# Kernel tuning notes

Hardware: AMD Instinct MI355X
Metric: run time of the kernel (lower is better)

The kernel has to match this reference:

```python
import jax, jax.numpy as jnp
import numpy as np

NUM_HEADS = 16
THETA = 10000.0


def _apply_rope(x, pos):
    # x: [b, h, t, d_k], pos: [t] int
    d = x.shape[-1]
    inv_freq = THETA ** (-jnp.arange(0, d, 2, dtype=jnp.float32) / d)  # [d/2]
    ang = pos.astype(jnp.float32)[:, None] * inv_freq                  # [t, d/2]
    cos, sin = jnp.cos(ang), jnp.sin(ang)
    x1, x2 = x[..., ::2], x[..., 1::2]
    r1 = x1 * cos - x2 * sin
    r2 = x1 * sin + x2 * cos
    return jnp.stack([r1, r2], axis=-1).reshape(x.shape)


def setup_inputs() -> dict:
    key = jax.random.key(0)
    k1, k2, k3 = jax.random.split(key, 3)
    b, t, dm = 4, 2048, 2048
    in_features = jax.random.normal(k1, (b, t, dm), dtype=jnp.float32)
    token_positions = jnp.arange(t, dtype=jnp.int64)
    W_qkv = jax.random.normal(k2, (3 * dm, dm), dtype=jnp.float32) * 0.02
    W_o = jax.random.normal(k3, (dm, dm), dtype=jnp.float32) * 0.02
    return {"in_features": in_features, "token_positions": token_positions,
            "W_qkv": W_qkv, "W_o": W_o}


def reference(in_features, token_positions, W_qkv, W_o):
    b, t, dm = in_features.shape
    h = NUM_HEADS
    dk = dm // h
    # fused QKV projection (Linear: y = x W^T)
    qkv = in_features @ W_qkv.T                       # [b, t, 3*dm]
    q, k, v = jnp.split(qkv, 3, axis=-1)
    def to_heads(x):
        return x.reshape(b, t, h, dk).transpose(0, 2, 1, 3)  # [b, h, t, dk]
    q, k, v = to_heads(q), to_heads(k), to_heads(v)
    q = _apply_rope(q, token_positions)
    k = _apply_rope(k, token_positions)
    # causal SDPA
    scale = 1.0 / np.sqrt(dk).astype(np.float32)
    scores = jnp.einsum('bhqd,bhkd->bhqk', q, k) * scale
    causal = jnp.tril(jnp.ones((t, t), dtype=bool))
    scores = jnp.where(causal, scores, jnp.finfo(scores.dtype).min)
    attn = jax.nn.softmax(scores, axis=-1)
    out = jnp.einsum('bhqk,bhkd->bhqd', attn, v)      # [b, h, t, dk]
    out = out.transpose(0, 2, 1, 3).reshape(b, t, dm)
    return out @ W_o.T
```

## Files before the change

### kernel.cpp

```cpp
#include <hip/hip_runtime.h>

typedef unsigned short u16;
typedef __attribute__((ext_vector_type(8))) short s8v;
typedef __attribute__((ext_vector_type(8))) __bf16 bf8;
typedef __attribute__((ext_vector_type(4))) float f4v;

#define GLB(p) ((const __attribute__((address_space(1))) void*)(p))
#define LDS(p) ((__attribute__((address_space(3))) void*)(p))

static __device__ __forceinline__ float b2f(u16 u) {
    union { unsigned int i; float f; } v; v.i = ((unsigned int)u) << 16; return v.f;
}
static __device__ __forceinline__ u16 f2b(float f) {
    union { float f; unsigned int i; } v; v.f = f;
    v.i += 0x7fffu + ((v.i >> 16) & 1u);
    return (u16)(v.i >> 16);
}

__global__ __launch_bounds__(256) void k_conv(const float* __restrict__ X,
                                              const float* __restrict__ Wq,
                                              const float* __restrict__ Wo,
                                              u16* __restrict__ Xb,
                                              u16* __restrict__ Wqb,
                                              u16* __restrict__ Wob) {
    int i = blockIdx.x * 256 + threadIdx.x;
    const float* in; u16* out; int off;
    if (i < 4194304)      { in = X;  out = Xb;  off = i; }
    else if (i < 7340032) { in = Wq; out = Wqb; off = i - 4194304; }
    else                  { in = Wo; out = Wob; off = i - 7340032; }
    float4 v = ((const float4*)in)[off];
    union { u16 u[4]; unsigned long long ll; } o;
    o.u[0] = f2b(v.x); o.u[1] = f2b(v.y); o.u[2] = f2b(v.z); o.u[3] = f2b(v.w);
    ((unsigned long long*)out)[off] = o.ll;
}

template<int MODE>
__global__ __launch_bounds__(512, 2) void k_gemm_bt(
    const u16* __restrict__ A, const u16* __restrict__ B,
    int K, int N, int gx,
    u16* __restrict__ Qb, u16* __restrict__ Kb, u16* __restrict__ Vt,
    float* __restrict__ Cf, const int* __restrict__ pos)
{
    extern __shared__ __align__(16) u16 Ls[];

    const int t    = threadIdx.x;
    const int lane = t & 63;
    const int wid  = t >> 6;
    const int wm = wid >> 2, wn = wid & 3;
    const int la = lane & 15, lb = lane >> 4;

    const int bid = (int)blockIdx.x;
    const int id2 = (bid & 7) * ((int)gridDim.x >> 3) + (bid >> 3);
    const int bx = id2 % gx, by = id2 / gx;
    const long arow0 = (long)by * 256;
    const long brow0 = (long)bx * 256;

    const int sr = t >> 3;
    const int sg = (t & 7) ^ (sr & 7);
    const u16* Asrc = A + (arow0 + sr) * (long)K + sg * 8;
    const u16* Bsrc = B + (brow0 + sr) * (long)K + sg * 8;
    const long K64 = 64 * (long)K, K128 = 128 * (long)K;
    u16* ldst = Ls + t * 8;

#define STG(q_, op_, h_, kt_) do {                                              \
        const u16* s_ = ((op_) ? Bsrc : Asrc) + (h_) * K128 + (long)(kt_) * 64; \
        u16* d_ = ldst + (q_) * 32768 + (op_) * 16384 + (h_) * 8192;            \
        __builtin_amdgcn_global_load_lds(GLB(s_),       LDS(d_),        16, 0, 0); \
        __builtin_amdgcn_global_load_lds(GLB(s_ + K64), LDS(d_ + 4096), 16, 0, 0); \
    } while (0)
#define RD(off) (*(const bf8*)(Ls + (off)))

    f4v acc[8][4];
#pragma unroll
    for (int m = 0; m < 8; m++)
#pragma unroll
        for (int n = 0; n < 4; n++) acc[m][n] = (f4v){0.f, 0.f, 0.f, 0.f};

    const int r7 = la & 7;
    const int gA0 = (lb ^ r7) * 8;
    const int gA1 = ((lb ^ r7) ^ 4) * 8;
    const int aRow = wm * 8192 + la * 64;
    const int bRow = 16384 + (wn >> 1) * 8192 + ((wn & 1) * 64 + la) * 64;

    const int NKT = K >> 6;
    STG(0, 0, 0, 0); STG(0, 0, 1, 0); STG(0, 1, 0, 0); STG(0, 1, 1, 0);
    asm volatile("s_waitcnt vmcnt(0)" ::: "memory");
    __builtin_amdgcn_s_barrier();

    for (int X = 0; X < NKT; ++X) {
        const int D = (X & 1) << 15;
        const int q = (X + 1) & 1;
        const int S = (X + 1 < NKT) ? X + 1 : NKT - 1;
        bf8 aR[4][2], b0[2][2], b1[2][2];

#pragma unroll
        for (int mi = 0; mi < 4; mi++) {
            aR[mi][0] = RD(D + aRow + mi * 1024 + gA0);
            aR[mi][1] = RD(D + aRow + mi * 1024 + gA1);
        }
#pragma unroll
        for (int nl = 0; nl < 2; nl++) {
            b0[nl][0] = RD(D + bRow + nl * 1024 + gA0);
            b0[nl][1] = RD(D + bRow + nl * 1024 + gA1);
        }
        STG(q, 0, 0, S); STG(q, 0, 1, S); STG(q, 1, 0, S); STG(q, 1, 1, S);
        __builtin_amdgcn_s_barrier();
        __builtin_amdgcn_s_setprio(1);
#pragma unroll
        for (int mi = 0; mi < 4; mi++)
#pragma unroll
            for (int nl = 0; nl < 2; nl++) {
                acc[mi][nl] = __builtin_amdgcn_mfma_f32_16x16x32_bf16(aR[mi][0], b0[nl][0], acc[mi][nl], 0, 0, 0);
                acc[mi][nl] = __builtin_amdgcn_mfma_f32_16x16x32_bf16(aR[mi][1], b0[nl][1], acc[mi][nl], 0, 0, 0);
            }
        __builtin_amdgcn_s_setprio(0);

#pragma unroll
        for (int nl = 0; nl < 2; nl++) {
            b1[nl][0] = RD(D + bRow + (2 + nl) * 1024 + gA0);
            b1[nl][1] = RD(D + bRow + (2 + nl) * 1024 + gA1);
        }
        __builtin_amdgcn_s_barrier();
        __builtin_amdgcn_s_setprio(1);
#pragma unroll
        for (int mi = 0; mi < 4; mi++)
#pragma unroll
            for (int nl = 0; nl < 2; nl++) {
                acc[mi][2 + nl] = __builtin_amdgcn_mfma_f32_16x16x32_bf16(aR[mi][0], b1[nl][0], acc[mi][2 + nl], 0, 0, 0);
                acc[mi][2 + nl] = __builtin_amdgcn_mfma_f32_16x16x32_bf16(aR[mi][1], b1[nl][1], acc[mi][2 + nl], 0, 0, 0);
            }
        __builtin_amdgcn_s_setprio(0);

#pragma unroll
        for (int mi = 0; mi < 4; mi++) {
            aR[mi][0] = RD(D + aRow + (4 + mi) * 1024 + gA0);
            aR[mi][1] = RD(D + aRow + (4 + mi) * 1024 + gA1);
        }
        __builtin_amdgcn_s_barrier();
        __builtin_amdgcn_s_setprio(1);
#pragma unroll
        for (int mi = 0; mi < 4; mi++)
#pragma unroll
            for (int nl = 0; nl < 2; nl++) {
                acc[4 + mi][2 + nl] = __builtin_amdgcn_mfma_f32_16x16x32_bf16(aR[mi][0], b1[nl][0], acc[4 + mi][2 + nl], 0, 0, 0);
                acc[4 + mi][2 + nl] = __builtin_amdgcn_mfma_f32_16x16x32_bf16(aR[mi][1], b1[nl][1], acc[4 + mi][2 + nl], 0, 0, 0);
            }
        __builtin_amdgcn_s_setprio(0);

        asm volatile("s_waitcnt vmcnt(0)" ::: "memory");
        __builtin_amdgcn_s_barrier();
        __builtin_amdgcn_s_setprio(1);
#pragma unroll
        for (int mi = 0; mi < 4; mi++)
#pragma unroll
            for (int nl = 0; nl < 2; nl++) {
                acc[4 + mi][nl] = __builtin_amdgcn_mfma_f32_16x16x32_bf16(aR[mi][0], b0[nl][0], acc[4 + mi][nl], 0, 0, 0);
                acc[4 + mi][nl] = __builtin_amdgcn_mfma_f32_16x16x32_bf16(aR[mi][1], b0[nl][1], acc[4 + mi][nl], 0, 0, 0);
            }
        __builtin_amdgcn_s_setprio(0);
    }
#undef STG
#undef RD

    if (MODE == 1) {
#pragma unroll
        for (int mi = 0; mi < 8; mi++)
#pragma unroll
            for (int ni = 0; ni < 4; ni++) {
                const long grow0 = arow0 + wm * 128 + mi * 16 + lb * 4;
                const int  gcol  = (int)brow0 + wn * 64 + ni * 16 + la;
#pragma unroll
                for (int i = 0; i < 4; i++)
                    Cf[(grow0 + i) * (long)N + gcol] = acc[mi][ni][i];
            }
        return;
    }

    __syncthreads();
    const int part = (int)(brow0 >> 11);
    const int colp = (int)brow0 & 2047;
    const int h0   = colp >> 7;
    const int bidx = (int)(arow0 >> 11);
    const int t0   = (int)arow0 & 2047;

    if (part == 2) {
#pragma unroll
        for (int mi = 0; mi < 8; mi++)
#pragma unroll
            for (int ni = 0; ni < 4; ni++) {
                const int tlb = wm * 128 + mi * 16 + lb * 4;
                const int dl  = wn * 64 + ni * 16 + la;
#pragma unroll
                for (int i2 = 0; i2 < 2; i2++) {
                    unsigned int pk = (unsigned int)f2b(acc[mi][ni][i2 * 2])
                                    | ((unsigned int)f2b(acc[mi][ni][i2 * 2 + 1]) << 16);
                    *(unsigned int*)(Ls + dl * 264 + tlb + i2 * 2) = pk;
                }
            }
        __syncthreads();
#pragma unroll
        for (int j = 0; j < 16; j++) {
            const int dl = j * 16 + wid * 2 + (lane >> 5);
            const int c  = lane & 31;
            bf8 v = *(const bf8*)(Ls + dl * 264 + c * 8);
            const long bh = (long)(bidx * 16 + h0 + (dl >> 7));
            *(bf8*)(Vt + (bh << 18) + ((long)(dl & 127) << 11) + t0 + c * 8) = v;
        }
    } else {
        u16* dst = (part == 0) ? Qb : Kb;
#pragma unroll
        for (int mi = 0; mi < 8; mi++)
#pragma unroll
            for (int ni = 0; ni < 4; ni++) {
                const int tlb = wm * 128 + mi * 16 + lb * 4;
                const int dl  = wn * 64 + ni * 16 + la;
#pragma unroll
                for (int i = 0; i < 4; i++)
                    Ls[(tlb + i) * 264 + dl] = f2b(acc[mi][ni][i]);
            }
        __syncthreads();
        const int c = t & 15;
        float invf[4];
#pragma unroll
        for (int p2 = 0; p2 < 4; p2++)
            invf[p2] = exp2f((float)(c * 4 + p2) * -0.20762050593046014f);
#pragma unroll
        for (int j = 0; j < 16; j++) {
            const int R  = j * 32 + (t >> 4);
            const int tl = R >> 1, hh = R & 1;
            s8v v = *(const s8v*)(Ls + tl * 264 + hh * 128 + c * 8);
            const float pf = (float)pos[t0 + tl];
            union { u16 u[8]; s8v v; } ov;
#pragma unroll
            for (int p2 = 0; p2 < 4; p2++) {
                float x1 = b2f((u16)v[2 * p2]);
                float x2 = b2f((u16)v[2 * p2 + 1]);
                float sn, cs;
                __sincosf(pf * invf[p2], &sn, &cs);
                ov.u[2 * p2]     = f2b(x1 * cs - x2 * sn);
                ov.u[2 * p2 + 1] = f2b(x1 * sn + x2 * cs);
            }
            const long bh = (long)(bidx * 16 + h0 + hh);
            *(s8v*)(dst + ((bh << 11) + t0 + tl) * 128 + c * 8) = ov.v;
        }
    }
}

__global__ __launch_bounds__(256) void k_attn(const u16* __restrict__ Qb,
                                              const u16* __restrict__ Kb,
                                              const u16* __restrict__ Vt,
                                              u16* __restrict__ Ob)
{
    extern __shared__ __align__(16) u16 Sm[];
    u16* KsD = Sm;
    u16* VsD = Sm + 16384;
    u16* PlD = Sm + 32768;

    const int tid  = threadIdx.x;
    const int lane = tid & 63;
    const int w    = tid >> 6;
    const int la = lane & 15, lb = lane >> 4;
    const int qg = 15 - ((int)blockIdx.x >> 6);
    const int bh = blockIdx.x & 63;
    const long base = (long)bh << 18;
    const int qt = qg * 4 + w;
    const int q0 = qt * 32;
    const int n32 = qt + 1;
    const int NT = qg * 2 + 2;
    const float scale = 0.08838834764831845f;

    bf8 qf[2][4];
#pragma unroll
    for (int m = 0; m < 2; m++)
#pragma unroll
        for (int kb = 0; kb < 4; kb++)
            qf[m][kb] = *(const bf8*)(Qb + base + (long)(q0 + m * 16 + la) * 128 + kb * 32 + lb * 8);

    f4v o[2][8];
#pragma unroll
    for (int m = 0; m < 2; m++)
#pragma unroll
        for (int n = 0; n < 8; n++) o[m][n] = (f4v){0.f, 0.f, 0.f, 0.f};
    float lst[2][4];
#pragma unroll
    for (int m = 0; m < 2; m++)
#pragma unroll
        for (int i = 0; i < 4; i++) lst[m][i] = 0.f;

    char* Pb = (char*)(PlD + w * 1024);

    const int krow = tid >> 4;
    const int kgr  = (tid & 15) ^ (krow & 7);
    const int vrow = tid >> 3;
    const int vgr  = (tid & 7) ^ (vrow & 7);

#define STAGE(buf, jt_) do {                                                         \
        const int kv0_ = (jt_) * 64;                                                \
        _Pragma("unroll")                                                           \
        for (int i_ = 0; i_ < 4; i_++) {                                            \
            __builtin_amdgcn_global_load_lds(                                       \
                GLB(Kb + base + (long)(kv0_ + i_ * 16 + krow) * 128 + kgr * 8),     \
                LDS(KsD + (buf) * 8192 + i_ * 2048 + tid * 8), 16, 0, 0);           \
            __builtin_amdgcn_global_load_lds(                                       \
                GLB(Vt + base + (long)(i_ * 32 + vrow) * 2048 + kv0_ + vgr * 8),    \
                LDS(VsD + (buf) * 8192 + i_ * 2048 + tid * 8), 16, 0, 0);           \
        }                                                                           \
    } while (0)

    STAGE(0, 0);

    for (int jt = 0; jt < NT; ++jt) {
        const int buf = jt & 1;
        asm volatile("s_waitcnt vmcnt(0)" ::: "memory");
        __builtin_amdgcn_s_barrier();
        if (jt + 1 < NT) STAGE(buf ^ 1, jt + 1);

        const u16* KsB = KsD + buf * 8192;
        const u16* VsB = VsD + buf * 8192;

#pragma unroll
        for (int h = 0; h < 2; h++) {
            const int j32 = jt * 2 + h;
            if (j32 < n32) {
                f4v s[2][2];
                s[0][0] = s[0][1] = s[1][0] = s[1][1] = (f4v){0.f, 0.f, 0.f, 0.f};
#pragma unroll
                for (int n = 0; n < 2; n++) {
                    const int rr = h * 32 + n * 16 + la;
#pragma unroll
                    for (int kb = 0; kb < 4; kb++) {
                        bf8 kf = *(const bf8*)(KsB + rr * 128 + (((kb * 4 + lb) ^ (la & 7)) * 8));
                        s[0][n] = __builtin_amdgcn_mfma_f32_16x16x32_bf16(qf[0][kb], kf, s[0][n], 0, 0, 0);
                        s[1][n] = __builtin_amdgcn_mfma_f32_16x16x32_bf16(qf[1][kb], kf, s[1][n], 0, 0, 0);
                    }
                }

                bf8 vf[8];
#pragma unroll
                for (int nO = 0; nO < 8; nO++) {
                    const int rv = nO * 16 + la;
                    vf[nO] = *(const bf8*)(VsB + rv * 64 + (((h * 4 + lb) ^ (la & 7)) * 8));
                }

                const bool diag = (j32 == qt);
                float p[2][2][4];
#pragma unroll
                for (int m = 0; m < 2; m++)
#pragma unroll
                    for (int n = 0; n < 2; n++)
#pragma unroll
                        for (int i = 0; i < 4; i++) {
                            float v = __expf(fmaf(s[m][n][i], scale, -8.0f));
                            if (diag && (n * 16 + la) > (m * 16 + lb * 4 + i)) v = 0.f;
                            p[m][n][i] = v;
                            lst[m][i] += v;
                        }

#pragma unroll
                for (int m = 0; m < 2; m++)
#pragma unroll
                    for (int n = 0; n < 2; n++)
#pragma unroll
                        for (int i = 0; i < 4; i++) {
                            const int row = m * 16 + lb * 4 + i;
                            const int colb = (n * 16 + la) * 2;
                            *(u16*)(Pb + row * 64 + (colb ^ ((row & 3) << 4))) = f2b(p[m][n][i]);
                        }
                bf8 pa[2];
#pragma unroll
                for (int am = 0; am < 2; am++) {
                    const int row = am * 16 + la;
                    pa[am] = *(const bf8*)(Pb + row * 64 + ((lb * 16) ^ ((row & 3) << 4)));
                }
#pragma unroll
                for (int nO = 0; nO < 8; nO++) {
                    o[0][nO] = __builtin_amdgcn_mfma_f32_16x16x32_bf16(pa[0], vf[nO], o[0][nO], 0, 0, 0);
                    o[1][nO] = __builtin_amdgcn_mfma_f32_16x16x32_bf16(pa[1], vf[nO], o[1][nO], 0, 0, 0);
                }
            }
        }
        __builtin_amdgcn_s_barrier();
    }
#undef STAGE

    float linv[2][4];
#pragma unroll
    for (int m = 0; m < 2; m++)
#pragma unroll
        for (int i = 0; i < 4; i++) {
            float l = lst[m][i];
            l += __shfl_xor(l, 1);
            l += __shfl_xor(l, 2);
            l += __shfl_xor(l, 4);
            l += __shfl_xor(l, 8);
            linv[m][i] = 1.0f / l;
        }

    const int b = bh >> 4, h = bh & 15;
#pragma unroll
    for (int m = 0; m < 2; m++)
#pragma unroll
        for (int nO = 0; nO < 8; nO++)
#pragma unroll
            for (int i = 0; i < 4; i++) {
                const int row = q0 + m * 16 + lb * 4 + i;
                const int d = nO * 16 + la;
                Ob[((long)(b * 2048 + row) << 11) + h * 128 + d] = f2b(o[m][nO][i] * linv[m][i]);
            }
}

extern "C" void kernel_launch(void* const* d_in, const int* in_sizes, int n_in,
                              void* d_out, int out_size, void* d_ws, size_t ws_size,
                              hipStream_t stream)
{
    const float* X    = (const float*)d_in[0];
    const int*   pos  = (const int*)d_in[1];
    const float* Wqkv = (const float*)d_in[2];
    const float* Wo   = (const float*)d_in[3];
    float* out = (float*)d_out;

    char* ws = (char*)d_ws;
    u16* Xb    = (u16*)(ws + 0);
    u16* Wqkvb = (u16*)(ws + 33554432);
    u16* Wob   = (u16*)(ws + 58720256);
    u16* Qb    = (u16*)(ws + 67108864);
    u16* Kb    = (u16*)(ws + 100663296);
    u16* Vt    = (u16*)(ws + 134217728);
    u16* Ob    = (u16*)(ws + 167772160);

    k_conv<<<32768, 256, 0, stream>>>(X, Wqkv, Wo, Xb, Wqkvb, Wob);
    k_gemm_bt<0><<<768, 512, 135168, stream>>>(Xb, Wqkvb, 2048, 6144, 24, Qb, Kb, Vt, nullptr, pos);
    k_attn<<<1024, 256, 73728, stream>>>(Qb, Kb, Vt, Ob);
    k_gemm_bt<1><<<256, 512, 131072, stream>>>(Ob, Wob, 2048, 2048, 8, nullptr, nullptr, nullptr, out, nullptr);
}
```

Measured before the change: 392.9 us.

## Simplify GEMM main loop to single-barrier double buffer with full fragment loads

Replaces the four-phase ping-pong GEMM K-loop, which interleaved partial LDS fragment reads with MFMA groups across several barriers, with a simpler scheme. Each iteration waits for the previous prefetch, does one barrier, issues the next tile's global-to-LDS loads, reads all A/B fragments, then runs all 64 MFMAs. It also drops a trailing barrier in the attention loop. This cuts barrier count and simplifies scheduling, but uses more registers for fragments, overlaps LDS reads with MFMA less, and removing the attention barrier could introduce an LDS race.

```diff
diff --git a/kernel.cpp b/kernel.cpp
--- a/kernel.cpp
+++ b/kernel.cpp
@@ -84,81 +84,38 @@
 
     const int NKT = K >> 6;
     STG(0, 0, 0, 0); STG(0, 0, 1, 0); STG(0, 1, 0, 0); STG(0, 1, 1, 0);
-    asm volatile("s_waitcnt vmcnt(0)" ::: "memory");
-    __builtin_amdgcn_s_barrier();
 
     for (int X = 0; X < NKT; ++X) {
-        const int D = (X & 1) << 15;
-        const int q = (X + 1) & 1;
-        const int S = (X + 1 < NKT) ? X + 1 : NKT - 1;
-        bf8 aR[4][2], b0[2][2], b1[2][2];
-
-#pragma unroll
-        for (int mi = 0; mi < 4; mi++) {
-            aR[mi][0] = RD(D + aRow + mi * 1024 + gA0);
-            aR[mi][1] = RD(D + aRow + mi * 1024 + gA1);
-        }
-#pragma unroll
-        for (int nl = 0; nl < 2; nl++) {
-            b0[nl][0] = RD(D + bRow + nl * 1024 + gA0);
-            b0[nl][1] = RD(D + bRow + nl * 1024 + gA1);
-        }
-        STG(q, 0, 0, S); STG(q, 0, 1, S); STG(q, 1, 0, S); STG(q, 1, 1, S);
-        __builtin_amdgcn_s_barrier();
-        __builtin_amdgcn_s_setprio(1);
-#pragma unroll
-        for (int mi = 0; mi < 4; mi++)
-#pragma unroll
-            for (int nl = 0; nl < 2; nl++) {
-                acc[mi][nl] = __builtin_amdgcn_mfma_f32_16x16x32_bf16(aR[mi][0], b0[nl][0], acc[mi][nl], 0, 0, 0);
-                acc[mi][nl] = __builtin_amdgcn_mfma_f32_16x16x32_bf16(aR[mi][1], b0[nl][1], acc[mi][nl], 0, 0, 0);
-            }
-        __builtin_amdgcn_s_setprio(0);
-
-#pragma unroll
-        for (int nl = 0; nl < 2; nl++) {
-            b1[nl][0] = RD(D + bRow + (2 + nl) * 1024 + gA0);
-            b1[nl][1] = RD(D + bRow + (2 + nl) * 1024 + gA1);
-        }
-        __builtin_amdgcn_s_barrier();
-        __builtin_amdgcn_s_setprio(1);
-#pragma unroll
-        for (int mi = 0; mi < 4; mi++)
-#pragma unroll
-            for (int nl = 0; nl < 2; nl++) {
-                acc[mi][2 + nl] = __builtin_amdgcn_mfma_f32_16x16x32_bf16(aR[mi][0], b1[nl][0], acc[mi][2 + nl], 0, 0, 0);
-                acc[mi][2 + nl] = __builtin_amdgcn_mfma_f32_16x16x32_bf16(aR[mi][1], b1[nl][1], acc[mi][2 + nl], 0, 0, 0);
-            }
-        __builtin_amdgcn_s_setprio(0);
-
-#pragma unroll
-        for (int mi = 0; mi < 4; mi++) {
-            aR[mi][0] = RD(D + aRow + (4 + mi) * 1024 + gA0);
-            aR[mi][1] = RD(D + aRow + (4 + mi) * 1024 + gA1);
-        }
-        __builtin_amdgcn_s_barrier();
-        __builtin_amdgcn_s_setprio(1);
-#pragma unroll
-        for (int mi = 0; mi < 4; mi++)
-#pragma unroll
-            for (int nl = 0; nl < 2; nl++) {
-                acc[4 + mi][2 + nl] = __builtin_amdgcn_mfma_f32_16x16x32_bf16(aR[mi][0], b1[nl][0], acc[4 + mi][2 + nl], 0, 0, 0);
-                acc[4 + mi][2 + nl] = __builtin_amdgcn_mfma_f32_16x16x32_bf16(aR[mi][1], b1[nl][1], acc[4 + mi][2 + nl], 0, 0, 0);
-            }
-        __builtin_amdgcn_s_setprio(0);
-
         asm volatile("s_waitcnt vmcnt(0)" ::: "memory");
         __builtin_amdgcn_s_barrier();
+        if (X + 1 < NKT) {
+            const int q = (X + 1) & 1;
+            STG(q, 0, 0, X + 1); STG(q, 0, 1, X + 1);
+            STG(q, 1, 0, X + 1); STG(q, 1, 1, X + 1);
+        }
+
+        const int D = (X & 1) << 15;
+        bf8 aF[8][2], bF[4][2];
+#pragma unroll
+        for (int mi = 0; mi < 8; mi++) aF[mi][0] = RD(D + aRow + mi * 1024 + gA0);
+#pragma unroll
+        for (int ni = 0; ni < 4; ni++) bF[ni][0] = RD(D + bRow + ni * 1024 + gA0);
+#pragma unroll
+        for (int mi = 0; mi < 8; mi++) aF[mi][1] = RD(D + aRow + mi * 1024 + gA1);
+#pragma unroll
+        for (int ni = 0; ni < 4; ni++) bF[ni][1] = RD(D + bRow + ni * 1024 + gA1);
+
         __builtin_amdgcn_s_setprio(1);
 #pragma unroll
-        for (int mi = 0; mi < 4; mi++)
-#pragma unroll
-            for (int nl = 0; nl < 2; nl++) {
-                acc[4 + mi][nl] = __builtin_amdgcn_mfma_f32_16x16x32_bf16(aR[mi][0], b0[nl][0], acc[4 + mi][nl], 0, 0, 0);
-                acc[4 + mi][nl] = __builtin_amdgcn_mfma_f32_16x16x32_bf16(aR[mi][1], b0[nl][1], acc[4 + mi][nl], 0, 0, 0);
-            }
+        for (int kk = 0; kk < 2; kk++)
+#pragma unroll
+            for (int mi = 0; mi < 8; mi++)
+#pragma unroll
+                for (int ni = 0; ni < 4; ni++)
+                    acc[mi][ni] = __builtin_amdgcn_mfma_f32_16x16x32_bf16(aF[mi][kk], bF[ni][kk], acc[mi][ni], 0, 0, 0);
         __builtin_amdgcn_s_setprio(0);
     }
+    asm volatile("s_waitcnt vmcnt(0)" ::: "memory");
 #undef STG
 #undef RD
 
@@ -379,7 +336,6 @@
                 }
             }
         }
-        __builtin_amdgcn_s_barrier();
     }
 #undef STAGE
 
```

Result: no change. 393.7 us (+0.2%).

## Load K/V fragments directly from global memory in attention, dropping LDS staging

Applied to the files above, without the earlier changes.

The attention kernel no longer stages K and V tiles into double-buffered shared memory with async global-to-LDS loads and block barriers. Each wave now reads its MFMA K and V fragments straight from global memory and walks its own causal range of 32-key tiles with no block-level synchronisation. This frees about 64KB of LDS per block to raise occupancy and removes barrier stalls between waves of uneven length. The cost is that the four waves of a block each fetch the same K/V data separately through the cache, with no software prefetch overlap.

```diff
diff --git a/kernel.cpp b/kernel.cpp
--- a/kernel.cpp
+++ b/kernel.cpp
@@ -251,10 +251,7 @@
                                               const u16* __restrict__ Vt,
                                               u16* __restrict__ Ob)
 {
-    extern __shared__ __align__(16) u16 Sm[];
-    u16* KsD = Sm;
-    u16* VsD = Sm + 16384;
-    u16* PlD = Sm + 32768;
+    __shared__ __align__(16) u16 Pl[4][1024];
 
     const int tid  = threadIdx.x;
     const int lane = tid & 63;
@@ -266,7 +263,6 @@
     const int qt = qg * 4 + w;
     const int q0 = qt * 32;
     const int n32 = qt + 1;
-    const int NT = qg * 2 + 2;
     const float scale = 0.08838834764831845f;
 
     bf8 qf[2][4];
@@ -287,101 +283,66 @@
 #pragma unroll
         for (int i = 0; i < 4; i++) lst[m][i] = 0.f;
 
-    char* Pb = (char*)(PlD + w * 1024);
-
-    const int krow = tid >> 4;
-    const int kgr  = (tid & 15) ^ (krow & 7);
-    const int vrow = tid >> 3;
-    const int vgr  = (tid & 7) ^ (vrow & 7);
-
-#define STAGE(buf, jt_) do {                                                         \
-        const int kv0_ = (jt_) * 64;                                                \
-        _Pragma("unroll")                                                           \
-        for (int i_ = 0; i_ < 4; i_++) {                                            \
-            __builtin_amdgcn_global_load_lds(                                       \
-                GLB(Kb + base + (long)(kv0_ + i_ * 16 + krow) * 128 + kgr * 8),     \
-                LDS(KsD + (buf) * 8192 + i_ * 2048 + tid * 8), 16, 0, 0);           \
-            __builtin_amdgcn_global_load_lds(                                       \
-                GLB(Vt + base + (long)(i_ * 32 + vrow) * 2048 + kv0_ + vgr * 8),    \
-                LDS(VsD + (buf) * 8192 + i_ * 2048 + tid * 8), 16, 0, 0);           \
-        }                                                                           \
-    } while (0)
-
-    STAGE(0, 0);
-
-    for (int jt = 0; jt < NT; ++jt) {
-        const int buf = jt & 1;
-        asm volatile("s_waitcnt vmcnt(0)" ::: "memory");
-        __builtin_amdgcn_s_barrier();
-        if (jt + 1 < NT) STAGE(buf ^ 1, jt + 1);
-
-        const u16* KsB = KsD + buf * 8192;
-        const u16* VsB = VsD + buf * 8192;
-
-#pragma unroll
-        for (int h = 0; h < 2; h++) {
-            const int j32 = jt * 2 + h;
-            if (j32 < n32) {
-                f4v s[2][2];
-                s[0][0] = s[0][1] = s[1][0] = s[1][1] = (f4v){0.f, 0.f, 0.f, 0.f};
-#pragma unroll
-                for (int n = 0; n < 2; n++) {
-                    const int rr = h * 32 + n * 16 + la;
-#pragma unroll
-                    for (int kb = 0; kb < 4; kb++) {
-                        bf8 kf = *(const bf8*)(KsB + rr * 128 + (((kb * 4 + lb) ^ (la & 7)) * 8));
-                        s[0][n] = __builtin_amdgcn_mfma_f32_16x16x32_bf16(qf[0][kb], kf, s[0][n], 0, 0, 0);
-                        s[1][n] = __builtin_amdgcn_mfma_f32_16x16x32_bf16(qf[1][kb], kf, s[1][n], 0, 0, 0);
-                    }
+    char* Pb = (char*)(Pl[w]);
+    const u16* Kg = Kb + base + (long)la * 128 + lb * 8;
+    const u16* Vg = Vt + base + (long)la * 2048 + lb * 8;
+
+    for (int j32 = 0; j32 < n32; ++j32) {
+        const int kv0 = j32 * 32;
+
+        bf8 vf[8];
+#pragma unroll
+        for (int nO = 0; nO < 8; nO++)
+            vf[nO] = *(const bf8*)(Vg + nO * 32768 + kv0);
+
+        f4v s[2][2];
+        s[0][0] = s[0][1] = s[1][0] = s[1][1] = (f4v){0.f, 0.f, 0.f, 0.f};
+#pragma unroll
+        for (int n = 0; n < 2; n++) {
+#pragma unroll
+            for (int kb = 0; kb < 4; kb++) {
+                bf8 kf = *(const bf8*)(Kg + (long)(kv0 + n * 16) * 128 + kb * 32);
+                s[0][n] = __builtin_amdgcn_mfma_f32_16x16x32_bf16(qf[0][kb], kf, s[0][n], 0, 0, 0);
+                s[1][n] = __builtin_amdgcn_mfma_f32_16x16x32_bf16(qf[1][kb], kf, s[1][n], 0, 0, 0);
+            }
+        }
+
+        const bool diag = (j32 == qt);
+        float p[2][2][4];
+#pragma unroll
+        for (int m = 0; m < 2; m++)
+#pragma unroll
+            for (int n = 0; n < 2; n++)
+#pragma unroll
+                for (int i = 0; i < 4; i++) {
+                    float v = __expf(fmaf(s[m][n][i], scale, -8.0f));
+                    if (diag && (n * 16 + la) > (m * 16 + lb * 4 + i)) v = 0.f;
+                    p[m][n][i] = v;
+                    lst[m][i] += v;
                 }
 
-                bf8 vf[8];
-#pragma unroll
-                for (int nO = 0; nO < 8; nO++) {
-                    const int rv = nO * 16 + la;
-                    vf[nO] = *(const bf8*)(VsB + rv * 64 + (((h * 4 + lb) ^ (la & 7)) * 8));
+#pragma unroll
+        for (int m = 0; m < 2; m++)
+#pragma unroll
+            for (int n = 0; n < 2; n++)
+#pragma unroll
+                for (int i = 0; i < 4; i++) {
+                    const int row = m * 16 + lb * 4 + i;
+                    const int colb = (n * 16 + la) * 2;
+                    *(u16*)(Pb + row * 64 + (colb ^ ((row & 3) << 4))) = f2b(p[m][n][i]);
                 }
-
-                const bool diag = (j32 == qt);
-                float p[2][2][4];
-#pragma unroll
-                for (int m = 0; m < 2; m++)
-#pragma unroll
-                    for (int n = 0; n < 2; n++)
-#pragma unroll
-                        for (int i = 0; i < 4; i++) {
-                            float v = __expf(fmaf(s[m][n][i], scale, -8.0f));
-                            if (diag && (n * 16 + la) > (m * 16 + lb * 4 + i)) v = 0.f;
-                            p[m][n][i] = v;
-                            lst[m][i] += v;
-                        }
-
-#pragma unroll
-                for (int m = 0; m < 2; m++)
-#pragma unroll
-                    for (int n = 0; n < 2; n++)
-#pragma unroll
-                        for (int i = 0; i < 4; i++) {
-                            const int row = m * 16 + lb * 4 + i;
-                            const int colb = (n * 16 + la) * 2;
-                            *(u16*)(Pb + row * 64 + (colb ^ ((row & 3) << 4))) = f2b(p[m][n][i]);
-                        }
-                bf8 pa[2];
-#pragma unroll
-                for (int am = 0; am < 2; am++) {
-                    const int row = am * 16 + la;
-                    pa[am] = *(const bf8*)(Pb + row * 64 + ((lb * 16) ^ ((row & 3) << 4)));
-                }
-#pragma unroll
-                for (int nO = 0; nO < 8; nO++) {
-                    o[0][nO] = __builtin_amdgcn_mfma_f32_16x16x32_bf16(pa[0], vf[nO], o[0][nO], 0, 0, 0);
-                    o[1][nO] = __builtin_amdgcn_mfma_f32_16x16x32_bf16(pa[1], vf[nO], o[1][nO], 0, 0, 0);
-                }
-            }
-        }
-        __builtin_amdgcn_s_barrier();
+        bf8 pa[2];
+#pragma unroll
+        for (int am = 0; am < 2; am++) {
+            const int row = am * 16 + la;
+            pa[am] = *(const bf8*)(Pb + row * 64 + ((lb * 16) ^ ((row & 3) << 4)));
+        }
+#pragma unroll
+        for (int nO = 0; nO < 8; nO++) {
+            o[0][nO] = __builtin_amdgcn_mfma_f32_16x16x32_bf16(pa[0], vf[nO], o[0][nO], 0, 0, 0);
+            o[1][nO] = __builtin_amdgcn_mfma_f32_16x16x32_bf16(pa[1], vf[nO], o[1][nO], 0, 0, 0);
+        }
     }
-#undef STAGE
 
     float linv[2][4];
 #pragma unroll
@@ -430,6 +391,6 @@
 
     k_conv<<<32768, 256, 0, stream>>>(X, Wqkv, Wo, Xb, Wqkvb, Wob);
     k_gemm_bt<0><<<768, 512, 135168, stream>>>(Xb, Wqkvb, 2048, 6144, 24, Qb, Kb, Vt, nullptr, pos);
-    k_attn<<<1024, 256, 73728, stream>>>(Qb, Kb, Vt, Ob);
+    k_attn<<<1024, 256, 0, stream>>>(Qb, Kb, Vt, Ob);
     k_gemm_bt<1><<<256, 512, 131072, stream>>>(Ob, Wob, 2048, 2048, 8, nullptr, nullptr, nullptr, out, nullptr);
 }
```

Measured after the change: 519.4 us. 32.2% more time.
